# Optimization experiments

Measured on AMD Instinct MI355X. Metric: run time of the kernel, lower is better.

The kernel has to match this reference:

```python
import jax, jax.numpy as jnp
import numpy as np


def _refl_conv(x, w, b, pad, stride):
    # ReflectionPad2d(pad) followed by Conv2d(stride=stride), NCHW / OIHW layouts.
    x = jnp.pad(x, ((0, 0), (0, 0), (pad, pad), (pad, pad)), mode='reflect')
    y = jax.lax.conv_general_dilated(
        x, w, window_strides=(stride, stride), padding='VALID',
        dimension_numbers=('NCHW', 'OIHW', 'NCHW'))
    return y + b[None, :, None, None]


def setup_inputs() -> dict:
    key = jax.random.key(0)
    ks = jax.random.split(key, 16)
    B, C, H, W = 8, 128, 64, 64
    IH, IW = 4 * H, 4 * W
    g = 0.02  # init gain ('normal' init in source)
    f32 = jnp.float32
    return {
        'feature_in': jax.random.normal(ks[0], (B, C, H, W), f32),
        'imgs': jax.random.uniform(ks[1], (B, 3, IH, IW), dtype=f32),
        'masks': jax.random.uniform(ks[2], (B, 1, IH, IW), dtype=f32),
        # Gate conv stack params (torch OIHW layout), biases zero per init_weights
        'gw1': g * jax.random.normal(ks[3], (32, 4, 7, 7), f32),
        'gb1': jnp.zeros((32,), f32),
        'gw2': g * jax.random.normal(ks[4], (64, 32, 5, 5), f32),
        'gb2': jnp.zeros((64,), f32),
        'gw3': g * jax.random.normal(ks[5], (128, 64, 5, 5), f32),
        'gb3': jnp.zeros((128,), f32),
        'gw4': g * jax.random.normal(ks[6], (256, 128, 3, 3), f32),
        'gb4': jnp.zeros((256,), f32),
        'gw5': g * jax.random.normal(ks[7], (1, 256, 3, 3), f32),
        'gb5': jnp.zeros((1,), f32),
        # combiner: Conv2d(2C -> C, 1x1)
        'cw': g * jax.random.normal(ks[8], (C, 2 * C, 1, 1), f32),
        'cb': jnp.zeros((C,), f32),
    }


def reference(feature_in, imgs, masks, gw1, gb1, gw2, gb2, gw3, gb3,
              gw4, gb4, gw5, gb5, cw, cb):
    PI = 3.1415926
    # ---- Gate ----
    x = jnp.concatenate([imgs, masks], axis=1)          # [B,4,4H,4W]
    s = jax.nn.relu(_refl_conv(x, gw1, gb1, 3, 1))
    s = jax.nn.relu(_refl_conv(s, gw2, gb2, 2, 2))
    s = jax.nn.relu(_refl_conv(s, gw3, gb3, 2, 1))
    s = jax.nn.relu(_refl_conv(s, gw4, gb4, 1, 2))
    s = jax.nn.relu(_refl_conv(s, gw5, gb5, 1, 1))      # [B,1,H,W]
    s = jnp.tan(PI * (jnp.tanh(s) - 0.5))
    B, C, H, W = feature_in.shape
    P = H * W
    gate = s.reshape(B, P, 1, 1)                        # row-major pixel order
    # ---- Att (patch_size=1: kernels are per-pixel feature vectors) ----
    K = feature_in.reshape(B, C, P).transpose(0, 2, 1) + 1e-7   # [B,P,C]
    Kn = K / jnp.sqrt(jnp.sum(K * K, axis=-1, keepdims=True))
    # attention_scores = conv2d(feature_map, K_norm) == cosine-like similarity
    scores = jnp.einsum('bpc,bcyx->bpyx', Kn, feature_in) + gate  # [B,P,H,W]
    A = jax.nn.softmax(scores, axis=1)
    # conv_transpose2d with 1x1 kernels == weighted sum of (unnormalized) kernels
    att = jnp.einsum('bpyx,bpc->bcyx', A, K)            # [B,C,H,W]
    # ---- combiner (1x1 conv on concat) ----
    cat = jnp.concatenate([att, feature_in], axis=1)    # [B,2C,H,W]
    out = jnp.einsum('oc,bcyx->boyx', cw[:, :, 0, 0], cat) + cb[None, :, None, None]
    return out
```

## Files before the change

kernel.cpp:

```cpp
#include <hip/hip_runtime.h>
#include <hip/hip_bf16.h>
#include <hip/hip_fp16.h>
#include <math.h>


#define PI_F 3.1415926f

typedef __attribute__((ext_vector_type(8))) short short8;
typedef __attribute__((ext_vector_type(4))) float f32x4;
typedef _Float16 half8 __attribute__((ext_vector_type(8)));
typedef __attribute__((ext_vector_type(4))) unsigned short u16x4;
typedef unsigned short ushort_t;

__device__ __forceinline__ ushort_t f2bf(float x) {
    unsigned u = __float_as_uint(x);
    unsigned r = (u + 0x7FFFu + ((u >> 16) & 1u)) >> 16;
    return (ushort_t)r;
}
__device__ __forceinline__ void split16(float x, ushort_t& h, ushort_t& l) {
    __half hh = __float2half(x);
    h = __half_as_ushort(hh);
    l = __half_as_ushort(__float2half(x - __half2float(hh)));
}
__device__ __forceinline__ ushort_t f2h(float x) {
    return __half_as_ushort(__float2half(x));
}
__device__ __forceinline__ int swz(int r, int c) {
    return ((c ^ r ^ (r >> 2)) & 3) << 3;
}

__global__ __launch_bounds__(256) void transform_w_k(
    const float* __restrict__ w, ushort_t* __restrict__ Wh, ushort_t* __restrict__ Wl,
    int Cout, int Cin, int KK)
{
    int idx = blockIdx.x * 256 + threadIdx.x;
    int N = Cout * Cin * KK;
    if (idx >= N) return;
    int oc = idx / (Cin * KK);
    int rem = idx - oc * (Cin * KK);
    int ic = rem / KK;
    int t = rem - ic * KK;
    float v = w[idx];
    long dst = ((long)t * Cout + oc) * Cin + ic;
    split16(v, Wh[dst], Wl[dst]);
}

__global__ __launch_bounds__(256) void transform_w1_k(
    const float* __restrict__ w, ushort_t* __restrict__ Wh, ushort_t* __restrict__ Wl)
{
    int idx = blockIdx.x * 256 + threadIdx.x;
    if (idx >= 7 * 32 * 32) return;
    int ky = idx / 1024;
    int rem = idx - ky * 1024;
    int oc = rem >> 5;
    int k = rem & 31;
    float v = 0.f;
    if (k < 28) {
        int kx = k >> 2, ic = k & 3;
        v = w[((oc * 4 + ic) * 7 + ky) * 7 + kx];
    }
    split16(v, Wh[idx], Wl[idx]);
}

__global__ __launch_bounds__(256) void prep_in_k(
    const float* __restrict__ imgs, const float* __restrict__ masks,
    ushort_t* __restrict__ Xh)
{
    const int iy = blockIdx.x, b = blockIdx.y;
    int sy = iy - 3; if (sy < 0) sy = -sy; if (sy >= 256) sy = 510 - sy;
    const int rb = sy << 8;
    const float* i0 = imgs + (long)b * 3 * 65536;
    const float* mk = masks + (long)b * 65536;
    for (int x = threadIdx.x; x < 262; x += 256) {
        int sx = x - 3; if (sx < 0) sx = -sx; if (sx >= 256) sx = 510 - sx;
        u16x4 hv;
        hv[0] = f2h(i0[rb + sx]);
        hv[1] = f2h(i0[65536 + rb + sx]);
        hv[2] = f2h(i0[131072 + rb + sx]);
        hv[3] = f2h(mk[rb + sx]);
        long o = ((long)(b * 262 + iy) * 262 + x) * 4;
        *(u16x4*)&Xh[o] = hv;
    }
}

__global__ __launch_bounds__(256) void conv1_mfma_k(
    const ushort_t* __restrict__ Xinh,
    const ushort_t* __restrict__ W1h, const ushort_t* __restrict__ W1l,
    const float* __restrict__ bias, ushort_t* __restrict__ Oh)
{
    const int tid = threadIdx.x, lane = tid & 63, wid = tid >> 6;
    const int wm = wid & 1, wn = wid >> 1, l15 = lane & 15, quad = lane >> 4;
    const int ox0 = blockIdx.x * 64;
    const int oy = blockIdx.y, b = blockIdx.z;
    f32x4 acc[2];
    acc[0] = (f32x4){0.f, 0.f, 0.f, 0.f};
    acc[1] = (f32x4){0.f, 0.f, 0.f, 0.f};
#pragma unroll
    for (int ky = 0; ky < 7; ++ky) {
        long wo = (long)(ky * 32 + wm * 16 + l15) * 32 + quad * 8;
        half8 Ah = *(const half8*)&W1h[wo];
        half8 Al = *(const half8*)&W1l[wo];
        long xrow = ((long)(b * 262 + oy + ky) * 262 + ox0) * 4;
#pragma unroll
        for (int ni = 0; ni < 2; ++ni) {
            long xo = xrow + (wn * 32 + ni * 16 + l15) * 4 + quad * 8;
            half8 Bh = *(const half8*)&Xinh[xo];
            acc[ni] = __builtin_amdgcn_mfma_f32_16x16x32_f16(Ah, Bh, acc[ni], 0, 0, 0);
            acc[ni] = __builtin_amdgcn_mfma_f32_16x16x32_f16(Al, Bh, acc[ni], 0, 0, 0);
        }
    }
    const int ocf = wm * 16 + quad * 4;
    float4 bv = *(const float4*)&bias[ocf];
#pragma unroll
    for (int ni = 0; ni < 2; ++ni) {
        int n = ox0 + wn * 32 + ni * 16 + l15;
        u16x4 hv;
        hv[0] = f2h(fmaxf(acc[ni][0] + bv.x, 0.f));
        hv[1] = f2h(fmaxf(acc[ni][1] + bv.y, 0.f));
        hv[2] = f2h(fmaxf(acc[ni][2] + bv.z, 0.f));
        hv[3] = f2h(fmaxf(acc[ni][3] + bv.w, 0.f));
        long o = ((long)(b * 260 + oy + 2) * 260 + n + 2) * 32 + ocf;
        *(u16x4*)&Oh[o] = hv;
    }
}

__global__ __launch_bounds__(256) void pad_cl_k(
    ushort_t* __restrict__ Xh, int Hp, int Wp, int PAD, int C, int H, int W)
{
    const int iy = blockIdx.x, b = blockIdx.y;
    int t = iy - PAD; if (t < 0) t = -t; if (t >= H) t = 2 * H - 2 - t;
    const int iys = t + PAD;
    const long rowd = ((long)(b * Hp + iy) * Wp) * C;
    const long rows = ((long)(b * Hp + iys) * Wp) * C;
    const int nch = Wp * (C >> 3);
    for (int idx = threadIdx.x; idx < nch; idx += 256) {
        int x = idx / (C >> 3);
        int cg = (idx - x * (C >> 3)) << 3;
        int t2 = x - PAD; if (t2 < 0) t2 = -t2; if (t2 >= W) t2 = 2 * W - 2 - t2;
        int xs = t2 + PAD;
        if (xs == x && iys == iy) continue;
        *(int4*)&Xh[rowd + (long)x * C + cg] = *(const int4*)&Xh[rows + (long)xs * C + cg];
    }
}

template<int K, int S, int CIN, int CSTG, int MT, int NPX, bool WRITE_CL>
__global__ __launch_bounds__(256, 2) void conv_mfma_k(
    const ushort_t* __restrict__ Xh,
    const ushort_t* __restrict__ Wh, const ushort_t* __restrict__ Wl,
    const float* __restrict__ bias,
    int Hp, int Wp, int CoutT,
    ushort_t* __restrict__ Oh, int Hpn, int Wpn, int NP,
    float* __restrict__ Ofp)
{
    constexpr int WS = (NPX - 1) * S + K;
    constexpr int WS2 = (WS + 1) / 2;
    constexpr int MF = MT / 32;
    constexpr int NF = NPX / 32;
    __shared__ ushort_t Bsh[WS * CSTG];
    __shared__ ushort_t Ash[K * MT * CSTG];
    __shared__ ushort_t Asl[K * MT * CSTG];
    const int tid = threadIdx.x, lane = tid & 63, wid = tid >> 6;
    const int wm = wid & 1, wn = wid >> 1, l15 = lane & 15, quad = lane >> 4;
    const int bx = blockIdx.x, oy = blockIdx.y;
    const int NOC = CoutT / MT;
    const int ocg = blockIdx.z % NOC, b = blockIdx.z / NOC;
    const int ox0 = bx * NPX;

    f32x4 acc[MF][NF];
#pragma unroll
    for (int mi = 0; mi < MF; ++mi)
#pragma unroll
        for (int ni = 0; ni < NF; ++ni) acc[mi][ni] = (f32x4){0.f, 0.f, 0.f, 0.f};

#pragma unroll
    for (int ky = 0; ky < K; ++ky) {
        const long rowoff = ((long)(b * Hp + oy * S + ky) * Wp + ox0 * S) * CIN;
        for (int cs = 0; cs < CIN; cs += CSTG) {
            __syncthreads();
            constexpr int NCH = WS * CSTG / 8;
#pragma unroll
            for (int it = 0; it < (NCH + 255) / 256; ++it) {
                int flat = tid + it * 256;
                if (flat < NCH) {
                    int e0 = flat * 8;
                    int x = e0 / CSTG;
                    int cpos = (e0 - x * CSTG) >> 3;
                    int xs = (S == 1) ? x : ((x >> 1) + (x & 1) * WS2);
                    *(int4*)&Bsh[xs * CSTG + swz(xs, cpos)] =
                        *(const int4*)&Xh[rowoff + (long)x * CIN + cs + cpos * 8];
                }
            }
            constexpr int NW = K * MT * CSTG / 8;
#pragma unroll
            for (int it = 0; it < (NW + 255) / 256; ++it) {
                int flat = tid + it * 256;
                if (flat < NW) {
                    int e0 = flat * 8;
                    int kx = e0 / (MT * CSTG);
                    int rem = e0 - kx * MT * CSTG;
                    int oc = rem / CSTG;
                    int cpos = (rem - oc * CSTG) >> 3;
                    int arow = kx * MT + oc;
                    int dst = arow * CSTG + swz(arow, cpos);
                    long src = ((long)((ky * K + kx) * CoutT + ocg * MT + oc)) * CIN + cs + cpos * 8;
                    *(int4*)&Ash[dst] = *(const int4*)&Wh[src];
                    *(int4*)&Asl[dst] = *(const int4*)&Wl[src];
                }
            }
            __syncthreads();
#pragma unroll
            for (int kx = 0; kx < K; ++kx) {
                half8 Ah[MF], Al[MF], Bh[NF];
#pragma unroll
                for (int mi = 0; mi < MF; ++mi) {
                    int arow = kx * MT + wm * (MT / 2) + mi * 16 + l15;
                    int ao = arow * CSTG + swz(arow, quad);
                    Ah[mi] = *(const half8*)&Ash[ao];
                    Al[mi] = *(const half8*)&Asl[ao];
                }
#pragma unroll
                for (int ni = 0; ni < NF; ++ni) {
                    int m = wn * (NPX / 2) + ni * 16 + l15;
                    int xs = (S == 1) ? (m + kx) : (m + (kx >> 1) + (kx & 1) * WS2);
                    Bh[ni] = *(const half8*)&Bsh[xs * CSTG + swz(xs, quad)];
                }
#pragma unroll
                for (int mi = 0; mi < MF; ++mi)
#pragma unroll
                    for (int ni = 0; ni < NF; ++ni) {
                        acc[mi][ni] = __builtin_amdgcn_mfma_f32_16x16x32_f16(Ah[mi], Bh[ni], acc[mi][ni], 0, 0, 0);
                        acc[mi][ni] = __builtin_amdgcn_mfma_f32_16x16x32_f16(Al[mi], Bh[ni], acc[mi][ni], 0, 0, 0);
                    }
            }
        }
    }
#pragma unroll
    for (int ni = 0; ni < NF; ++ni) {
        const int n = ox0 + wn * (NPX / 2) + ni * 16 + l15;
#pragma unroll
        for (int mi = 0; mi < MF; ++mi) {
            const int ocf = ocg * MT + wm * (MT / 2) + mi * 16 + quad * 4;
            float4 bv = *(const float4*)&bias[ocf];
            float v0 = fmaxf(acc[mi][ni][0] + bv.x, 0.f);
            float v1 = fmaxf(acc[mi][ni][1] + bv.y, 0.f);
            float v2 = fmaxf(acc[mi][ni][2] + bv.z, 0.f);
            float v3 = fmaxf(acc[mi][ni][3] + bv.w, 0.f);
            if (WRITE_CL) {
                long o = ((long)(b * Hpn + oy + NP) * Wpn + n + NP) * CoutT + ocf;
                u16x4 hv;
                hv[0] = f2h(v0); hv[1] = f2h(v1); hv[2] = f2h(v2); hv[3] = f2h(v3);
                *(u16x4*)&Oh[o] = hv;
            } else {
                long o = ((long)(b * CoutT + ocf) << 12) + (oy << 6) + n;
                Ofp[o] = v0;
                Ofp[o + 4096] = v1;
                Ofp[o + 8192] = v2;
                Ofp[o + 12288] = v3;
            }
        }
    }
}

__global__ __launch_bounds__(256) void conv5_gate_k(
    const float* __restrict__ s4, const float* __restrict__ w,
    const float* __restrict__ bias, float* __restrict__ gate)
{
    const int tid = threadIdx.x;
    const int lane = tid & 63, g = tid >> 6;
    const int oy = blockIdx.x, b = blockIdx.y;
    int ixo[3], iyo[3];
#pragma unroll
    for (int k = 0; k < 3; ++k) {
        int ix = lane + k - 1; if (ix < 0) ix = -ix; if (ix >= 64) ix = 126 - ix;
        int iy = oy + k - 1; if (iy < 0) iy = -iy; if (iy >= 64) iy = 126 - iy;
        ixo[k] = ix; iyo[k] = iy << 6;
    }
    float part = 0.f;
    const float* inb = s4 + ((long)b * 256 + g * 64) * 4096;
    const float* wg = w + g * 64 * 9;
    for (int ic = 0; ic < 64; ++ic) {
        const float* inc = inb + ic * 4096;
        const float* wc = wg + ic * 9;
#pragma unroll
        for (int ky = 0; ky < 3; ++ky)
#pragma unroll
            for (int kx = 0; kx < 3; ++kx)
                part = fmaf(wc[ky * 3 + kx], inc[iyo[ky] + ixo[kx]], part);
    }
    __shared__ float red[4][64];
    red[g][lane] = part;
    __syncthreads();
    if (tid < 64) {
        float s = bias[0] + red[0][tid] + red[1][tid] + red[2][tid] + red[3][tid];
        s = fmaxf(s, 0.f);
        gate[(b << 12) + (oy << 6) + tid] = tanf(PI_F * (tanhf(s) - 0.5f));
    }
}

__global__ __launch_bounds__(256) void invn_k(const float* __restrict__ F, float* __restrict__ invn)
{
    const int p = blockIdx.x * 256 + threadIdx.x;
    const int b = blockIdx.y;
    const float* Fb = F + (long)b * 524288;
    float ss = 0.f;
#pragma unroll 8
    for (int c = 0; c < 128; ++c) {
        float v = Fb[c * 4096 + p] + 1e-7f;
        ss = fmaf(v, v, ss);
    }
    invn[(b << 12) + p] = 1.0f / sqrtf(ss);
}

__global__ __launch_bounds__(256) void prep_bf16_k(
    const float* __restrict__ F, ushort_t* __restrict__ Fo16, ushort_t* __restrict__ Ft16)
{
    __shared__ float Ls[128][65];
    const int tid = threadIdx.x;
    const int lane = tid & 63, wv = tid >> 6;
    const int p0 = blockIdx.x * 64, b = blockIdx.y;
#pragma unroll 8
    for (int cc = 0; cc < 32; ++cc) {
        int c = wv * 32 + cc;
        long idx = ((long)b * 128 + c) * 4096 + p0 + lane;
        float v = F[idx];
        Fo16[idx] = f2bf(v);
        Ls[c][lane] = v;
    }
    __syncthreads();
#pragma unroll 8
    for (int i = 0; i < 32; ++i) {
        int flat = tid + 256 * i;
        int c = flat & 127, pl_ = flat >> 7;
        Ft16[((long)b * 4096 + p0 + pl_) * 128 + c] = f2bf(Ls[c][pl_]);
    }
}

__global__ __launch_bounds__(64, 1) void flash_attn_k(
    const ushort_t* __restrict__ Ft16, const ushort_t* __restrict__ Fo16,
    const float* __restrict__ invn, const float* __restrict__ gate,
    float* __restrict__ Opart, float* __restrict__ lpart)
{
    const int lane = threadIdx.x & 63;
    const int l15 = lane & 15, quad = lane >> 4;
    const int b = blockIdx.x;
    const int qb = blockIdx.y & 63, ks = blockIdx.y >> 6;
    const int q0 = qb * 64;
    const int bp = b << 12;
    const ushort_t* Ftb = Ft16 + (long)b * 4096 * 128;
    const ushort_t* Fob = Fo16 + (long)b * 128 * 4096;

    short8 Bq[4][4];
#pragma unroll
    for (int ni = 0; ni < 4; ++ni)
#pragma unroll
        for (int cs = 0; cs < 4; ++cs)
            Bq[ni][cs] = *(const short8*)&Ftb[(long)(q0 + ni * 16 + l15) * 128 + cs * 32 + quad * 8];

    f32x4 O[8][4];
#pragma unroll
    for (int ct = 0; ct < 8; ++ct)
#pragma unroll
        for (int ni = 0; ni < 4; ++ni) O[ct][ni] = (f32x4){0.f, 0.f, 0.f, 0.f};
    float l_acc[4] = {0.f, 0.f, 0.f, 0.f};

    union BeU { short8 v; __hip_bfloat162 h[4]; };
    const int p_beg = ks * 1024;
    const int prow_base = ((l15 & 12) << 1) + (l15 & 3);

    short8 Ap[2][2][4];
    short8 Va[2][8];
    float4 ivb[2][2], gtb[2][2];

    {
        const int p0w = p_beg;
#pragma unroll
        for (int sub = 0; sub < 2; ++sub) {
            const long prow = p0w + prow_base + sub * 4;
#pragma unroll
            for (int cs = 0; cs < 4; ++cs)
                Ap[0][sub][cs] = *(const short8*)&Ftb[prow * 128 + cs * 32 + quad * 8];
            ivb[0][sub] = *(const float4*)&invn[bp + p0w + quad * 8 + sub * 4];
            gtb[0][sub] = *(const float4*)&gate[bp + p0w + quad * 8 + sub * 4];
        }
#pragma unroll
        for (int ct = 0; ct < 8; ++ct)
            Va[0][ct] = *(const short8*)&Fob[(long)(ct * 16 + l15) * 4096 + p0w + quad * 8];
    }

#pragma unroll 2
    for (int t = 0; t < 32; ++t) {
        const int cur = t & 1, nxt = cur ^ 1;
        if (t + 1 < 32) {
            const int p1 = p_beg + (t + 1) * 32;
#pragma unroll
            for (int sub = 0; sub < 2; ++sub) {
                const long prow = p1 + prow_base + sub * 4;
#pragma unroll
                for (int cs = 0; cs < 4; ++cs)
                    Ap[nxt][sub][cs] = *(const short8*)&Ftb[prow * 128 + cs * 32 + quad * 8];
                ivb[nxt][sub] = *(const float4*)&invn[bp + p1 + quad * 8 + sub * 4];
                gtb[nxt][sub] = *(const float4*)&gate[bp + p1 + quad * 8 + sub * 4];
            }
#pragma unroll
            for (int ct = 0; ct < 8; ++ct)
                Va[nxt][ct] = *(const short8*)&Fob[(long)(ct * 16 + l15) * 4096 + p1 + quad * 8];
        }
        BeU be[4];
#pragma unroll
        for (int sub = 0; sub < 2; ++sub) {
            f32x4 Sa[4];
#pragma unroll
            for (int ni = 0; ni < 4; ++ni) Sa[ni] = (f32x4){0.f, 0.f, 0.f, 0.f};
#pragma unroll
            for (int cs = 0; cs < 4; ++cs)
#pragma unroll
                for (int ni = 0; ni < 4; ++ni)
                    Sa[ni] = __builtin_amdgcn_mfma_f32_16x16x32_bf16(Ap[cur][sub][cs], Bq[ni][cs], Sa[ni], 0, 0, 0);
            const float4 iv = ivb[cur][sub];
            const float4 gt = gtb[cur][sub];
#pragma unroll
            for (int ni = 0; ni < 4; ++ni) {
                float e0 = __expf(fmaf(Sa[ni][0], iv.x, gt.x));
                float e1 = __expf(fmaf(Sa[ni][1], iv.y, gt.y));
                float e2 = __expf(fmaf(Sa[ni][2], iv.z, gt.z));
                float e3 = __expf(fmaf(Sa[ni][3], iv.w, gt.w));
                be[ni].h[sub * 2]     = __float22bfloat162_rn(make_float2(e0, e1));
                be[ni].h[sub * 2 + 1] = __float22bfloat162_rn(make_float2(e2, e3));
                l_acc[ni] += (e0 + e1) + (e2 + e3);
            }
        }
#pragma unroll
        for (int ct = 0; ct < 8; ++ct)
#pragma unroll
            for (int ni = 0; ni < 4; ++ni)
                O[ct][ni] = __builtin_amdgcn_mfma_f32_16x16x32_bf16(Va[cur][ct], be[ni].v, O[ct][ni], 0, 0, 0);
    }

#pragma unroll
    for (int ni = 0; ni < 4; ++ni) {
        float lt = l_acc[ni];
        lt += __shfl_xor(lt, 16);
        lt += __shfl_xor(lt, 32);
        if (quad == 0)
            lpart[(ks * 8 + b) * 4096 + q0 + ni * 16 + l15] = lt;
    }
    float* Ob = Opart + (long)(ks * 8 + b) * 524288;
#pragma unroll
    for (int ct = 0; ct < 8; ++ct)
#pragma unroll
        for (int ni = 0; ni < 4; ++ni) {
            int c = ct * 16 + quad * 4;
            int q = q0 + ni * 16 + l15;
#pragma unroll
            for (int r = 0; r < 4; ++r)
                Ob[((long)(c + r) << 12) + q] = O[ct][ni][r];
        }
}

__global__ __launch_bounds__(256) void combiner_k(
    const float* __restrict__ Opart, const float* __restrict__ lpart,
    const float* __restrict__ F, const float* __restrict__ cw,
    const float* __restrict__ cb, float* __restrict__ out)
{
    const int tid = threadIdx.x;
    const int q = blockIdx.x * 256 + tid;
    const int o0 = blockIdx.y << 4;
    const int b = blockIdx.z;
    float lsum = 0.f;
#pragma unroll
    for (int ks = 0; ks < 4; ++ks) lsum += lpart[(ks * 8 + b) * 4096 + q];
    float il = 1.0f / lsum;
    const float* Fb = F + (long)b * 524288 + q;
    float acc[16];
#pragma unroll
    for (int j = 0; j < 16; ++j) acc[j] = cb[o0 + j];
    for (int c = 0; c < 128; ++c) {
        float a = 0.f;
#pragma unroll
        for (int ks = 0; ks < 4; ++ks)
            a += Opart[(long)(ks * 8 + b) * 524288 + (long)c * 4096 + q];
        a *= il;
        float f = Fb[(long)c * 4096];
#pragma unroll
        for (int j = 0; j < 16; ++j) {
            acc[j] = fmaf(cw[(o0 + j) * 256 + c], a, acc[j]);
            acc[j] = fmaf(cw[(o0 + j) * 256 + 128 + c], f, acc[j]);
        }
    }
#pragma unroll
    for (int j = 0; j < 16; ++j)
        out[((long)(b * 128 + o0 + j) << 12) + q] = acc[j];
}

extern "C" void kernel_launch(void* const* d_in, const int* in_sizes, int n_in,
                              void* d_out, int out_size, void* d_ws, size_t ws_size,
                              hipStream_t stream)
{
    const float* F     = (const float*)d_in[0];
    const float* imgs  = (const float*)d_in[1];
    const float* masks = (const float*)d_in[2];
    const float* gw1 = (const float*)d_in[3];  const float* gb1 = (const float*)d_in[4];
    const float* gw2 = (const float*)d_in[5];  const float* gb2 = (const float*)d_in[6];
    const float* gw3 = (const float*)d_in[7];  const float* gb3 = (const float*)d_in[8];
    const float* gw4 = (const float*)d_in[9];  const float* gb4 = (const float*)d_in[10];
    const float* gw5 = (const float*)d_in[11]; const float* gb5 = (const float*)d_in[12];
    const float* cw  = (const float*)d_in[13]; const float* cb  = (const float*)d_in[14];
    float* out = (float*)d_out;

    float* W = (float*)d_ws;
    ushort_t* Xcl2h = (ushort_t*)(W);
    ushort_t* Xcl4h = (ushort_t*)(W);
    float*    Opart = W;
    float*    lpart = W + 16777216;
    ushort_t* Xcl3h = (ushort_t*)(W + 17305600);
    ushort_t* Fo16  = (ushort_t*)(W + 17305600);
    float*    s4   = W + 26226688;
    ushort_t* Ft16 = (ushort_t*)(W + 30420992);
    ushort_t* W2h = (ushort_t*)(W + 34615296);
    ushort_t* W2l = (ushort_t*)(W + 34640896);
    ushort_t* W3h = (ushort_t*)(W + 34666496);
    ushort_t* W3l = (ushort_t*)(W + 34768896);
    ushort_t* W4h = (ushort_t*)(W + 34871296);
    ushort_t* W4l = (ushort_t*)(W + 35018752);
    float* gate = W + 35166208;
    float* invn = W + 35198976;
    ushort_t* Xinh = (ushort_t*)(W + 35231744);
    ushort_t* W1h  = (ushort_t*)(W + 37428416);
    ushort_t* W1l  = (ushort_t*)(W + 37432000);

    transform_w_k<<<dim3(200),  256, 0, stream>>>(gw2, W2h, W2l, 64, 32, 25);
    transform_w_k<<<dim3(800),  256, 0, stream>>>(gw3, W3h, W3l, 128, 64, 25);
    transform_w_k<<<dim3(1152), 256, 0, stream>>>(gw4, W4h, W4l, 256, 128, 9);
    transform_w1_k<<<dim3(28), 256, 0, stream>>>(gw1, W1h, W1l);
    prep_in_k<<<dim3(262, 8), 256, 0, stream>>>(imgs, masks, Xinh);

    conv1_mfma_k<<<dim3(4, 256, 8), 256, 0, stream>>>(Xinh, W1h, W1l, gb1, Xcl2h);
    pad_cl_k<<<dim3(260, 8), 256, 0, stream>>>(Xcl2h, 260, 260, 2, 32, 256, 256);
    conv_mfma_k<5, 2, 32, 32, 64, 128, true><<<dim3(1, 128, 8), 256, 0, stream>>>(
        Xcl2h, W2h, W2l, gb2, 260, 260, 64, Xcl3h, 132, 132, 2, nullptr);
    pad_cl_k<<<dim3(132, 8), 256, 0, stream>>>(Xcl3h, 132, 132, 2, 64, 128, 128);
    conv_mfma_k<5, 1, 64, 32, 64, 128, true><<<dim3(1, 128, 16), 256, 0, stream>>>(
        Xcl3h, W3h, W3l, gb3, 132, 132, 128, Xcl4h, 130, 130, 1, nullptr);
    pad_cl_k<<<dim3(130, 8), 256, 0, stream>>>(Xcl4h, 130, 130, 1, 128, 128, 128);
    conv_mfma_k<3, 2, 128, 32, 128, 64, false><<<dim3(1, 64, 16), 256, 0, stream>>>(
        Xcl4h, W4h, W4l, gb4, 130, 130, 256, nullptr, 0, 0, 0, s4);
    conv5_gate_k<<<dim3(64, 8), 256, 0, stream>>>(s4, gw5, gb5, gate);

    invn_k<<<dim3(16, 8), 256, 0, stream>>>(F, invn);
    prep_bf16_k<<<dim3(64, 8), 256, 0, stream>>>(F, Fo16, Ft16);
    flash_attn_k<<<dim3(8, 256, 1), 64, 0, stream>>>(Ft16, Fo16, invn, gate, Opart, lpart);
    combiner_k<<<dim3(16, 8, 8), 256, 0, stream>>>(Opart, lpart, F, cw, cb, out);
}
```

Baseline: 632.9 us.

## Halve flash-attention query tile and drop V/scale prefetch to raise occupancy

```diff
diff --git a/kernel.cpp b/kernel.cpp
--- a/kernel.cpp
+++ b/kernel.cpp
@@ -335,7 +335,7 @@
     }
 }
 
-__global__ __launch_bounds__(64, 1) void flash_attn_k(
+__global__ __launch_bounds__(64, 2) void flash_attn_k(
     const ushort_t* __restrict__ Ft16, const ushort_t* __restrict__ Fo16,
     const float* __restrict__ invn, const float* __restrict__ gate,
     float* __restrict__ Opart, float* __restrict__ lpart)
@@ -343,101 +343,96 @@
     const int lane = threadIdx.x & 63;
     const int l15 = lane & 15, quad = lane >> 4;
     const int b = blockIdx.x;
-    const int qb = blockIdx.y & 63, ks = blockIdx.y >> 6;
-    const int q0 = qb * 64;
+    const int qb = blockIdx.y & 127, ks = blockIdx.y >> 7;
+    const int q0 = qb * 32;
     const int bp = b << 12;
     const ushort_t* Ftb = Ft16 + (long)b * 4096 * 128;
     const ushort_t* Fob = Fo16 + (long)b * 128 * 4096;
 
-    short8 Bq[4][4];
-#pragma unroll
-    for (int ni = 0; ni < 4; ++ni)
+    short8 Bq[2][4];
+#pragma unroll
+    for (int ni = 0; ni < 2; ++ni)
 #pragma unroll
         for (int cs = 0; cs < 4; ++cs)
             Bq[ni][cs] = *(const short8*)&Ftb[(long)(q0 + ni * 16 + l15) * 128 + cs * 32 + quad * 8];
 
-    f32x4 O[8][4];
+    f32x4 O[8][2];
 #pragma unroll
     for (int ct = 0; ct < 8; ++ct)
 #pragma unroll
-        for (int ni = 0; ni < 4; ++ni) O[ct][ni] = (f32x4){0.f, 0.f, 0.f, 0.f};
-    float l_acc[4] = {0.f, 0.f, 0.f, 0.f};
+        for (int ni = 0; ni < 2; ++ni) O[ct][ni] = (f32x4){0.f, 0.f, 0.f, 0.f};
+    float l_acc[2] = {0.f, 0.f};
 
     union BeU { short8 v; __hip_bfloat162 h[4]; };
     const int p_beg = ks * 1024;
     const int prow_base = ((l15 & 12) << 1) + (l15 & 3);
 
     short8 Ap[2][2][4];
-    short8 Va[2][8];
-    float4 ivb[2][2], gtb[2][2];
-
     {
-        const int p0w = p_beg;
 #pragma unroll
         for (int sub = 0; sub < 2; ++sub) {
-            const long prow = p0w + prow_base + sub * 4;
+            const long prow = p_beg + prow_base + sub * 4;
 #pragma unroll
             for (int cs = 0; cs < 4; ++cs)
                 Ap[0][sub][cs] = *(const short8*)&Ftb[prow * 128 + cs * 32 + quad * 8];
-            ivb[0][sub] = *(const float4*)&invn[bp + p0w + quad * 8 + sub * 4];
-            gtb[0][sub] = *(const float4*)&gate[bp + p0w + quad * 8 + sub * 4];
-        }
-#pragma unroll
-        for (int ct = 0; ct < 8; ++ct)
-            Va[0][ct] = *(const short8*)&Fob[(long)(ct * 16 + l15) * 4096 + p0w + quad * 8];
+        }
     }
 
 #pragma unroll 2
     for (int t = 0; t < 32; ++t) {
         const int cur = t & 1, nxt = cur ^ 1;
+        const int p0w = p_beg + t * 32;
         if (t + 1 < 32) {
-            const int p1 = p_beg + (t + 1) * 32;
+            const int p1 = p0w + 32;
 #pragma unroll
             for (int sub = 0; sub < 2; ++sub) {
                 const long prow = p1 + prow_base + sub * 4;
 #pragma unroll
                 for (int cs = 0; cs < 4; ++cs)
                     Ap[nxt][sub][cs] = *(const short8*)&Ftb[prow * 128 + cs * 32 + quad * 8];
-                ivb[nxt][sub] = *(const float4*)&invn[bp + p1 + quad * 8 + sub * 4];
-                gtb[nxt][sub] = *(const float4*)&gate[bp + p1 + quad * 8 + sub * 4];
-            }
-#pragma unroll
-            for (int ct = 0; ct < 8; ++ct)
-                Va[nxt][ct] = *(const short8*)&Fob[(long)(ct * 16 + l15) * 4096 + p1 + quad * 8];
-        }
-        BeU be[4];
+            }
+        }
+        short8 Va[8];
+#pragma unroll
+        for (int ct = 0; ct < 8; ++ct)
+            Va[ct] = *(const short8*)&Fob[(long)(ct * 16 + l15) * 4096 + p0w + quad * 8];
+        float4 iv[2], gt[2];
 #pragma unroll
         for (int sub = 0; sub < 2; ++sub) {
-            f32x4 Sa[4];
-#pragma unroll
-            for (int ni = 0; ni < 4; ++ni) Sa[ni] = (f32x4){0.f, 0.f, 0.f, 0.f};
-#pragma unroll
-            for (int cs = 0; cs < 4; ++cs)
-#pragma unroll
-                for (int ni = 0; ni < 4; ++ni)
-                    Sa[ni] = __builtin_amdgcn_mfma_f32_16x16x32_bf16(Ap[cur][sub][cs], Bq[ni][cs], Sa[ni], 0, 0, 0);
-            const float4 iv = ivb[cur][sub];
-            const float4 gt = gtb[cur][sub];
-#pragma unroll
-            for (int ni = 0; ni < 4; ++ni) {
-                float e0 = __expf(fmaf(Sa[ni][0], iv.x, gt.x));
-                float e1 = __expf(fmaf(Sa[ni][1], iv.y, gt.y));
-                float e2 = __expf(fmaf(Sa[ni][2], iv.z, gt.z));
-                float e3 = __expf(fmaf(Sa[ni][3], iv.w, gt.w));
+            iv[sub] = *(const float4*)&invn[bp + p0w + quad * 8 + sub * 4];
+            gt[sub] = *(const float4*)&gate[bp + p0w + quad * 8 + sub * 4];
+        }
+        BeU be[2];
+#pragma unroll
+        for (int sub = 0; sub < 2; ++sub) {
+            f32x4 Sa[2];
+            Sa[0] = (f32x4){0.f, 0.f, 0.f, 0.f};
+            Sa[1] = (f32x4){0.f, 0.f, 0.f, 0.f};
+#pragma unroll
+            for (int cs = 0; cs < 4; ++cs) {
+                Sa[0] = __builtin_amdgcn_mfma_f32_16x16x32_bf16(Ap[cur][sub][cs], Bq[0][cs], Sa[0], 0, 0, 0);
+                Sa[1] = __builtin_amdgcn_mfma_f32_16x16x32_bf16(Ap[cur][sub][cs], Bq[1][cs], Sa[1], 0, 0, 0);
+            }
+#pragma unroll
+            for (int ni = 0; ni < 2; ++ni) {
+                float e0 = __expf(fmaf(Sa[ni][0], iv[sub].x, gt[sub].x));
+                float e1 = __expf(fmaf(Sa[ni][1], iv[sub].y, gt[sub].y));
+                float e2 = __expf(fmaf(Sa[ni][2], iv[sub].z, gt[sub].z));
+                float e3 = __expf(fmaf(Sa[ni][3], iv[sub].w, gt[sub].w));
                 be[ni].h[sub * 2]     = __float22bfloat162_rn(make_float2(e0, e1));
                 be[ni].h[sub * 2 + 1] = __float22bfloat162_rn(make_float2(e2, e3));
                 l_acc[ni] += (e0 + e1) + (e2 + e3);
             }
         }
 #pragma unroll
-        for (int ct = 0; ct < 8; ++ct)
-#pragma unroll
-            for (int ni = 0; ni < 4; ++ni)
-                O[ct][ni] = __builtin_amdgcn_mfma_f32_16x16x32_bf16(Va[cur][ct], be[ni].v, O[ct][ni], 0, 0, 0);
-    }
-
-#pragma unroll
-    for (int ni = 0; ni < 4; ++ni) {
+        for (int ct = 0; ct < 8; ++ct) {
+            O[ct][0] = __builtin_amdgcn_mfma_f32_16x16x32_bf16(Va[ct], be[0].v, O[ct][0], 0, 0, 0);
+            O[ct][1] = __builtin_amdgcn_mfma_f32_16x16x32_bf16(Va[ct], be[1].v, O[ct][1], 0, 0, 0);
+        }
+    }
+
+#pragma unroll
+    for (int ni = 0; ni < 2; ++ni) {
         float lt = l_acc[ni];
         lt += __shfl_xor(lt, 16);
         lt += __shfl_xor(lt, 32);
@@ -448,7 +443,7 @@
 #pragma unroll
     for (int ct = 0; ct < 8; ++ct)
 #pragma unroll
-        for (int ni = 0; ni < 4; ++ni) {
+        for (int ni = 0; ni < 2; ++ni) {
             int c = ct * 16 + quad * 4;
             int q = q0 + ni * 16 + l15;
 #pragma unroll
@@ -548,6 +543,6 @@
 
     invn_k<<<dim3(16, 8), 256, 0, stream>>>(F, invn);
     prep_bf16_k<<<dim3(64, 8), 256, 0, stream>>>(F, Fo16, Ft16);
-    flash_attn_k<<<dim3(8, 256, 1), 64, 0, stream>>>(Ft16, Fo16, invn, gate, Opart, lpart);
+    flash_attn_k<<<dim3(8, 512, 1), 64, 0, stream>>>(Ft16, Fo16, invn, gate, Opart, lpart);
     combiner_k<<<dim3(16, 8, 8), 256, 0, stream>>>(Opart, lpart, F, cw, cb, out);
 }
```

Result: slower. 748.9 us (+18.3%).
